# Kernel tuning notes

Measured on AMD Instinct MI355X. Metric: run time of the kernel, lower is better.

The kernel has to match this reference:

```python
import jax, jax.numpy as jnp
import numpy as np

RES = 2048
STEPS = 65536
SIGMA = 0.01
W = 32  # source computes w from sigma then hardcodes w = 32


def setup_inputs() -> dict:
    key = jax.random.key(0)
    # 3 control points (x, y) in [0, 1]
    control_points = jax.random.uniform(key, (3, 2), dtype=jnp.float32)
    return {"control_points": control_points}


def reference(control_points):
    p0, p1, p2 = control_points[0], control_points[1], control_points[2]
    # lin_interp uses torch.linspace(0, 1, steps)
    t_lin = jnp.linspace(0.0, 1.0, STEPS, dtype=jnp.float32)  # [steps]
    a = p0[:, None] + (p1 - p0)[:, None] * t_lin  # [2, steps]
    b = p1[:, None] + (p2 - p1)[:, None] * t_lin  # [2, steps]
    # forward uses arange(steps)/steps (NOT linspace) for the outer blend
    t_out = jnp.arange(STEPS, dtype=jnp.float32) / float(STEPS)
    curve = a + t_out * (b - a)  # [2, steps]

    # per-step block corner indices (int -> non-differentiable, as in torch .int())
    blocks = jnp.clip(jnp.floor(RES * curve).astype(jnp.int32) - W // 2, 0, RES - W)  # [2, steps]
    bx, by = blocks[0], blocks[1]  # [steps]
    offs = jnp.arange(W, dtype=jnp.int32)

    # grid values inside each block: self.c[a,b,t] = a/res, self.d[a,b,t] = b/res
    ci = (bx[:, None] + offs).astype(jnp.float32) / float(RES)  # [steps, w]
    cj = (by[:, None] + offs).astype(jnp.float32) / float(RES)  # [steps, w]

    dx = curve[0][:, None] - ci  # [steps, w]
    dy = curve[1][:, None] - cj  # [steps, w]
    inv = 1.0 / (2.0 * SIGMA * SIGMA)
    patch = jnp.exp(-(dx[:, :, None] ** 2 + dy[:, None, :] ** 2) * inv)  # [steps, w, w]

    # scatter each step's patch into the grid; mean over steps == sum/steps
    ii = bx[:, None, None] + offs[None, :, None]  # [steps, w, 1] -> broadcast
    jj = by[:, None, None] + offs[None, None, :]  # [steps, 1, w]
    ii = jnp.broadcast_to(ii, (STEPS, W, W))
    jj = jnp.broadcast_to(jj, (STEPS, W, W))
    raster = jnp.zeros((RES, RES), dtype=jnp.float32).at[ii, jj].add(patch)
    return raster / float(STEPS)
```

## Files before the change

kernel.cpp:

```cpp
#include <hip/hip_runtime.h>
#include <hip/hip_bf16.h>

#define RES_    2048
#define CSTEPS  128
#define TILE_   48
#define KPAD    136
#define NTHR    576

typedef _Float16 half8 __attribute__((ext_vector_type(8)));
typedef float   float4_ __attribute__((ext_vector_type(4)));

__global__ __launch_bounds__(NTHR) void bezier_scatter(const float* __restrict__ cp,
                                                       float* __restrict__ out) {
    __shared__ _Float16 sExT[TILE_][KPAD];
    __shared__ _Float16 sEyT[TILE_][KPAD];
    __shared__ float s_cx[CSTEPS], s_cy[CSTEPS];
    __shared__ int   s_bx[CSTEPS], s_by[CSTEPS];
    __shared__ int   s_Ax, s_Ay;

    const int tid = threadIdx.x;

    if (tid < CSTEPS) {
        const int gs = blockIdx.x * CSTEPS + tid;
        const float tl = (float)((double)gs / 65535.0);
        const float to = (float)gs * (1.0f / 65536.0f);
        const float p0x = cp[0], p0y = cp[1], p1x = cp[2], p1y = cp[3], p2x = cp[4], p2y = cp[5];
        const float ax = __fadd_rn(p0x, __fmul_rn(__fsub_rn(p1x, p0x), tl));
        const float ay = __fadd_rn(p0y, __fmul_rn(__fsub_rn(p1y, p0y), tl));
        const float bxf = __fadd_rn(p1x, __fmul_rn(__fsub_rn(p2x, p1x), tl));
        const float byf = __fadd_rn(p1y, __fmul_rn(__fsub_rn(p2y, p1y), tl));
        const float cx = __fadd_rn(ax, __fmul_rn(to, __fsub_rn(bxf, ax)));
        const float cy = __fadd_rn(ay, __fmul_rn(to, __fsub_rn(byf, ay)));
        const int bxi = min(max((int)floorf(__fmul_rn(2048.0f, cx)) - 16, 0), RES_ - 32);
        const int byi = min(max((int)floorf(__fmul_rn(2048.0f, cy)) - 16, 0), RES_ - 32);
        s_cx[tid] = cx; s_cy[tid] = cy; s_bx[tid] = bxi; s_by[tid] = byi;
        if (tid == 0) {
            s_Ax = min(max(bxi - 8, 0), RES_ - TILE_);
            s_Ay = min(max(byi - 8, 0), RES_ - TILE_);
        }
    }
    __syncthreads();
    const int Ax = s_Ax, Ay = s_Ay;

    for (int it = tid; it < 2 * TILE_ * (CSTEPS / 8); it += NTHR) {
        const int half_ = TILE_ * (CSTEPS / 8);
        const int table = (it >= half_);
        const int rem   = it - table * half_;
        const int o     = rem >> 4;
        const int s0    = (rem & 15) * 8;
        const float* cc = table ? s_cy : s_cx;
        const int*   bb = table ? s_by : s_bx;
        const int  base = table ? Ay : Ax;
        const float ci  = (float)(base + o) * (1.0f / 2048.0f);
        half8 v;
        #pragma unroll
        for (int j = 0; j < 8; ++j) {
            const int s = s0 + j;
            const float d = __fsub_rn(cc[s], ci);
            const float e = __expf(-__fmul_rn(__fmul_rn(d, d), 5000.0f));
            const unsigned orel = (unsigned)(base + o - bb[s]);
            v[j] = (orel < 32u) ? (_Float16)e : (_Float16)0.0f;
        }
        *(half8*)(table ? &sEyT[o][s0] : &sExT[o][s0]) = v;
    }
    __syncthreads();

    const int lane = tid & 63;
    const int wid  = tid >> 6;
    const int mt   = wid / 3, nt = wid - mt * 3;
    const int arow = mt * 16 + (lane & 15);
    const int bcol = nt * 16 + (lane & 15);
    const int kgrp = (lane >> 4) * 8;
    float4_ acc = {0.f, 0.f, 0.f, 0.f};
    #pragma unroll
    for (int kb = 0; kb < CSTEPS / 32; ++kb) {
        const half8 aF = *(const half8*)&sExT[arow][kb * 32 + kgrp];
        const half8 bF = *(const half8*)&sEyT[bcol][kb * 32 + kgrp];
        acc = __builtin_amdgcn_mfma_f32_16x16x32_f16(aF, bF, acc, 0, 0, 0);
    }

    const int coll = lane & 15;
    const int rowb = (lane >> 4) * 4;
    #pragma unroll
    for (int r = 0; r < 4; ++r) {
        const float v = acc[r];
        if (v != 0.0f) {
            const int gx = Ax + mt * 16 + rowb + r;
            const int gy = Ay + nt * 16 + coll;
            atomicAdd(&out[gx * RES_ + gy], v * (1.0f / 65536.0f));
        }
    }
}

extern "C" void kernel_launch(void* const* d_in, const int* in_sizes, int n_in,
                              void* d_out, int out_size, void* d_ws, size_t ws_size,
                              hipStream_t stream) {
    const float* cp = (const float*)d_in[0];
    float* out = (float*)d_out;
    hipMemsetAsync(out, 0, (size_t)out_size * sizeof(float), stream);
    hipLaunchKernelGGL(bezier_scatter, dim3(65536 / CSTEPS), dim3(NTHR), 0, stream, cp, out);
}
```

Baseline: 21.35 us.

## Switch from per-chunk atomic scatter to per-output-tile gather with chunk culling

Replaces the step-chunk-parallel kernel, which atomically added 48x48 patches into a memset grid, with an output-tile-parallel kernel. Each of 4096 blocks owns a 32x32 tile, culls the 512 step chunks by bounding box, and accumulates the overlapping ones with MFMA. It writes the tile directly, which removes the memset and the atomics. The cost is uneven work: blocks far from the curve only write zeros, while blocks near it loop over several chunks with repeated barriers.

After: 45.48 us. +113.0%, slower.

```diff
diff --git a/kernel.cpp b/kernel.cpp
--- a/kernel.cpp
+++ b/kernel.cpp
@@ -1,95 +1,166 @@
 #include <hip/hip_runtime.h>
 #include <hip/hip_bf16.h>
 
-#define RES_    2048
-#define CSTEPS  128
-#define TILE_   48
-#define KPAD    136
-#define NTHR    576
+#define RES_   2048
+#define CH_    128
+#define NCH    512
+#define TS_    32
+#define KPAD   136
+#define NTHR   512
 
-typedef _Float16 half8 __attribute__((ext_vector_type(8)));
+typedef _Float16 half8  __attribute__((ext_vector_type(8)));
+typedef float   float2_ __attribute__((ext_vector_type(2)));
 typedef float   float4_ __attribute__((ext_vector_type(4)));
 
-__global__ __launch_bounds__(NTHR) void bezier_scatter(const float* __restrict__ cp,
-                                                       float* __restrict__ out) {
-    __shared__ _Float16 sExT[TILE_][KPAD];
-    __shared__ _Float16 sEyT[TILE_][KPAD];
-    __shared__ float s_cx[CSTEPS], s_cy[CSTEPS];
-    __shared__ int   s_bx[CSTEPS], s_by[CSTEPS];
-    __shared__ int   s_Ax, s_Ay;
+__device__ __forceinline__ void step_eval(int gs, float p0x, float p0y, float p1x, float p1y,
+                                          float p2x, float p2y, float& cx, float& cy) {
+    const float tl = (float)((double)gs / 65535.0);
+    const float to = (float)gs * (1.0f / 65536.0f);
+    const float ax  = __fadd_rn(p0x, __fmul_rn(__fsub_rn(p1x, p0x), tl));
+    const float ay  = __fadd_rn(p0y, __fmul_rn(__fsub_rn(p1y, p0y), tl));
+    const float bxf = __fadd_rn(p1x, __fmul_rn(__fsub_rn(p2x, p1x), tl));
+    const float byf = __fadd_rn(p1y, __fmul_rn(__fsub_rn(p2y, p1y), tl));
+    cx = __fadd_rn(ax, __fmul_rn(to, __fsub_rn(bxf, ax)));
+    cy = __fadd_rn(ay, __fmul_rn(to, __fsub_rn(byf, ay)));
+}
+
+__device__ __forceinline__ void step_eval_fast(int gs, float p0x, float p0y, float p1x, float p1y,
+                                               float p2x, float p2y, float& cx, float& cy) {
+    const float tl = (float)gs * (1.0f / 65535.0f);
+    const float to = (float)gs * (1.0f / 65536.0f);
+    const float ax  = p0x + (p1x - p0x) * tl;
+    const float ay  = p0y + (p1y - p0y) * tl;
+    const float bxf = p1x + (p2x - p1x) * tl;
+    const float byf = p1y + (p2y - p1y) * tl;
+    cx = ax + to * (bxf - ax);
+    cy = ay + to * (byf - ay);
+}
+
+__global__ __launch_bounds__(NTHR) void bezier_tiles(const float* __restrict__ cp,
+                                                     float* __restrict__ out) {
+    __shared__ _Float16 sExT[TS_][KPAD];
+    __shared__ _Float16 sEyT[TS_][KPAD];
+    __shared__ float    sOut[TS_][36];
+    __shared__ float    s_cx[CH_], s_cy[CH_];
+    __shared__ int      s_bx[CH_], s_by[CH_];
+    __shared__ unsigned short s_list[NCH];
+    __shared__ int      s_wcnt[8];
+    __shared__ int      s_count;
 
     const int tid = threadIdx.x;
+    const int bid = blockIdx.x;
+    const int Tx = (bid >> 6) * TS_;
+    const int Ty = (bid & 63) * TS_;
 
-    if (tid < CSTEPS) {
-        const int gs = blockIdx.x * CSTEPS + tid;
-        const float tl = (float)((double)gs / 65535.0);
-        const float to = (float)gs * (1.0f / 65536.0f);
-        const float p0x = cp[0], p0y = cp[1], p1x = cp[2], p1y = cp[3], p2x = cp[4], p2y = cp[5];
-        const float ax = __fadd_rn(p0x, __fmul_rn(__fsub_rn(p1x, p0x), tl));
-        const float ay = __fadd_rn(p0y, __fmul_rn(__fsub_rn(p1y, p0y), tl));
-        const float bxf = __fadd_rn(p1x, __fmul_rn(__fsub_rn(p2x, p1x), tl));
-        const float byf = __fadd_rn(p1y, __fmul_rn(__fsub_rn(p2y, p1y), tl));
-        const float cx = __fadd_rn(ax, __fmul_rn(to, __fsub_rn(bxf, ax)));
-        const float cy = __fadd_rn(ay, __fmul_rn(to, __fsub_rn(byf, ay)));
-        const int bxi = min(max((int)floorf(__fmul_rn(2048.0f, cx)) - 16, 0), RES_ - 32);
-        const int byi = min(max((int)floorf(__fmul_rn(2048.0f, cy)) - 16, 0), RES_ - 32);
-        s_cx[tid] = cx; s_cy[tid] = cy; s_bx[tid] = bxi; s_by[tid] = byi;
-        if (tid == 0) {
-            s_Ax = min(max(bxi - 8, 0), RES_ - TILE_);
-            s_Ay = min(max(byi - 8, 0), RES_ - TILE_);
-        }
+    const float p0x = cp[0], p0y = cp[1], p1x = cp[2], p1y = cp[3], p2x = cp[4], p2y = cp[5];
+
+    bool ov = false;
+    {
+        float x0, y0, x1, y1;
+        step_eval_fast(tid * CH_,           p0x,p0y,p1x,p1y,p2x,p2y, x0, y0);
+        step_eval_fast(tid * CH_ + CH_ - 1, p0x,p0y,p1x,p1y,p2x,p2y, x1, y1);
+        const int bxlo = min(max((int)floorf(2048.f * fminf(x0, x1)) - 18, 0), RES_ - 32);
+        const int bxhi = min(max((int)floorf(2048.f * fmaxf(x0, x1)) - 14, 0), RES_ - 32);
+        const int bylo = min(max((int)floorf(2048.f * fminf(y0, y1)) - 18, 0), RES_ - 32);
+        const int byhi = min(max((int)floorf(2048.f * fmaxf(y0, y1)) - 14, 0), RES_ - 32);
+        ov = (bxlo <= Tx + TS_ - 1) && (bxhi + 31 >= Tx) &&
+             (bylo <= Ty + TS_ - 1) && (byhi + 31 >= Ty);
+    }
+    const unsigned long long m = __ballot(ov ? 1 : 0);
+    const int lane = tid & 63;
+    const int w    = tid >> 6;
+    if (lane == 0) s_wcnt[w] = __popcll(m);
+    __syncthreads();
+    if (ov) {
+        int pre = 0;
+        for (int i = 0; i < w; ++i) pre += s_wcnt[i];
+        const int pos = pre + __popcll(m & ((1ull << lane) - 1ull));
+        s_list[pos] = (unsigned short)tid;
+    }
+    if (tid == 0) {
+        int t = 0;
+        for (int i = 0; i < 8; ++i) t += s_wcnt[i];
+        s_count = t;
     }
     __syncthreads();
-    const int Ax = s_Ax, Ay = s_Ay;
+    const int cnt = s_count;
 
-    for (int it = tid; it < 2 * TILE_ * (CSTEPS / 8); it += NTHR) {
-        const int half_ = TILE_ * (CSTEPS / 8);
-        const int table = (it >= half_);
-        const int rem   = it - table * half_;
-        const int o     = rem >> 4;
-        const int s0    = (rem & 15) * 8;
-        const float* cc = table ? s_cy : s_cx;
-        const int*   bb = table ? s_by : s_bx;
-        const int  base = table ? Ay : Ax;
-        const float ci  = (float)(base + o) * (1.0f / 2048.0f);
-        half8 v;
+    const int orow = tid >> 4;
+    const int oc2  = (tid & 15) * 2;
+    float* const orow_ptr = &out[(size_t)(Tx + orow) * RES_ + Ty + oc2];
+
+    if (cnt == 0) {
+        *(float2_*)orow_ptr = float2_{0.f, 0.f};
+        return;
+    }
+
+    const int st = w & 3;
+    const int kh = w >> 2;
+    const int mt = st >> 1, nt = st & 1;
+    const int arow = mt * 16 + (lane & 15);
+    const int bcol = nt * 16 + (lane & 15);
+    const int kg   = kh * 64 + (lane >> 4) * 8;
+    float4_ acc = {0.f, 0.f, 0.f, 0.f};
+
+    for (int p = 0; p < cnt; ++p) {
+        const int c = s_list[p];
+        if (tid < CH_) {
+            float cx, cy;
+            step_eval(c * CH_ + tid, p0x,p0y,p1x,p1y,p2x,p2y, cx, cy);
+            s_cx[tid] = cx; s_cy[tid] = cy;
+            s_bx[tid] = min(max((int)floorf(__fmul_rn(2048.0f, cx)) - 16, 0), RES_ - 32);
+            s_by[tid] = min(max((int)floorf(__fmul_rn(2048.0f, cy)) - 16, 0), RES_ - 32);
+        }
+        __syncthreads();
         #pragma unroll
-        for (int j = 0; j < 8; ++j) {
-            const int s = s0 + j;
-            const float d = __fsub_rn(cc[s], ci);
-            const float e = __expf(-__fmul_rn(__fmul_rn(d, d), 5000.0f));
-            const unsigned orel = (unsigned)(base + o - bb[s]);
-            v[j] = (orel < 32u) ? (_Float16)e : (_Float16)0.0f;
+        for (int rep = 0; rep < 2; ++rep) {
+            const int it    = tid + rep * NTHR;
+            const int table = it >> 9;
+            const int rem   = it & 511;
+            const int o     = rem >> 4;
+            const int s0    = (rem & 15) * 8;
+            const float* cc = table ? s_cy : s_cx;
+            const int*   bb = table ? s_by : s_bx;
+            const int  base = table ? Ty : Tx;
+            const float ci  = (float)(base + o) * (1.0f / 2048.0f);
+            half8 v;
+            #pragma unroll
+            for (int j = 0; j < 8; ++j) {
+                const int s = s0 + j;
+                const float d = __fsub_rn(cc[s], ci);
+                const float e = __expf(-__fmul_rn(__fmul_rn(d, d), 5000.0f));
+                const unsigned orel = (unsigned)(base + o - bb[s]);
+                v[j] = (orel < 32u) ? (_Float16)e : (_Float16)0.0f;
+            }
+            *(half8*)(table ? &sEyT[o][s0] : &sExT[o][s0]) = v;
         }
-        *(half8*)(table ? &sEyT[o][s0] : &sExT[o][s0]) = v;
+        __syncthreads();
+        #pragma unroll
+        for (int kb = 0; kb < 2; ++kb) {
+            const int k = kb * 32 + kg;
+            const half8 aF = *(const half8*)&sExT[arow][k];
+            const half8 bF = *(const half8*)&sEyT[bcol][k];
+            acc = __builtin_amdgcn_mfma_f32_16x16x32_f16(aF, bF, acc, 0, 0, 0);
+        }
+        __syncthreads();
+    }
+
+    const float sc = 1.0f / 65536.0f;
+    const int coll = lane & 15;
+    const int rowb = (lane >> 4) * 4;
+    if (kh == 0) {
+        #pragma unroll
+        for (int r = 0; r < 4; ++r)
+            sOut[mt * 16 + rowb + r][nt * 16 + coll] = acc[r] * sc;
     }
     __syncthreads();
-
-    const int lane = tid & 63;
-    const int wid  = tid >> 6;
-    const int mt   = wid / 3, nt = wid - mt * 3;
-    const int arow = mt * 16 + (lane & 15);
-    const int bcol = nt * 16 + (lane & 15);
-    const int kgrp = (lane >> 4) * 8;
-    float4_ acc = {0.f, 0.f, 0.f, 0.f};
-    #pragma unroll
-    for (int kb = 0; kb < CSTEPS / 32; ++kb) {
-        const half8 aF = *(const half8*)&sExT[arow][kb * 32 + kgrp];
-        const half8 bF = *(const half8*)&sEyT[bcol][kb * 32 + kgrp];
-        acc = __builtin_amdgcn_mfma_f32_16x16x32_f16(aF, bF, acc, 0, 0, 0);
+    if (kh == 1) {
+        #pragma unroll
+        for (int r = 0; r < 4; ++r)
+            sOut[mt * 16 + rowb + r][nt * 16 + coll] += acc[r] * sc;
     }
-
-    const int coll = lane & 15;
-    const int rowb = (lane >> 4) * 4;
-    #pragma unroll
-    for (int r = 0; r < 4; ++r) {
-        const float v = acc[r];
-        if (v != 0.0f) {
-            const int gx = Ax + mt * 16 + rowb + r;
-            const int gy = Ay + nt * 16 + coll;
-            atomicAdd(&out[gx * RES_ + gy], v * (1.0f / 65536.0f));
-        }
-    }
+    __syncthreads();
+    *(float2_*)orow_ptr = *(const float2_*)&sOut[orow][oc2];
 }
 
 extern "C" void kernel_launch(void* const* d_in, const int* in_sizes, int n_in,
@@ -97,6 +168,5 @@
                               hipStream_t stream) {
     const float* cp = (const float*)d_in[0];
     float* out = (float*)d_out;
-    hipMemsetAsync(out, 0, (size_t)out_size * sizeof(float), stream);
-    hipLaunchKernelGGL(bezier_scatter, dim3(65536 / CSTEPS), dim3(NTHR), 0, stream, cp, out);
+    hipLaunchKernelGGL(bezier_tiles, dim3(4096), dim3(NTHR), 0, stream, cp, out);
 }
```

## Replace memset plus atomic scatter with chunk tiles and a gather pass

Applied to the files above, without the earlier changes.

Each chunk block now writes its 48x48 partial tile and its tile origin to workspace instead of atomically adding into the output. A second kernel gives each 32x32 output tile one block, which ballot-compacts the overlapping chunks and sums their tile values, then writes every output element once. This removes the separate 16 MB memset and the atomic contention, at the cost of an extra launch and a full-grid write plus workspace reads. There is also some leftover dead code in the prefix loop.

Measured after the change: 36.93 us. +73.0%, slower.

```diff
diff --git a/kernel.cpp b/kernel.cpp
--- a/kernel.cpp
+++ b/kernel.cpp
@@ -3,15 +3,19 @@
 
 #define RES_    2048
 #define CSTEPS  128
+#define NCH     512
 #define TILE_   48
 #define KPAD    136
-#define NTHR    576
+#define NTHR1   576
+#define WSTILE  2304
+#define NTHR2   256
 
-typedef _Float16 half8 __attribute__((ext_vector_type(8)));
+typedef _Float16 half8  __attribute__((ext_vector_type(8)));
 typedef float   float4_ __attribute__((ext_vector_type(4)));
 
-__global__ __launch_bounds__(NTHR) void bezier_scatter(const float* __restrict__ cp,
-                                                       float* __restrict__ out) {
+__global__ __launch_bounds__(NTHR1) void bezier_chunks(const float* __restrict__ cp,
+                                                       float* __restrict__ wst,
+                                                       int* __restrict__ wsa) {
     __shared__ _Float16 sExT[TILE_][KPAD];
     __shared__ _Float16 sEyT[TILE_][KPAD];
     __shared__ float s_cx[CSTEPS], s_cy[CSTEPS];
@@ -37,12 +41,14 @@
         if (tid == 0) {
             s_Ax = min(max(bxi - 8, 0), RES_ - TILE_);
             s_Ay = min(max(byi - 8, 0), RES_ - TILE_);
+            wsa[2 * blockIdx.x]     = s_Ax;
+            wsa[2 * blockIdx.x + 1] = s_Ay;
         }
     }
     __syncthreads();
     const int Ax = s_Ax, Ay = s_Ay;
 
-    for (int it = tid; it < 2 * TILE_ * (CSTEPS / 8); it += NTHR) {
+    for (int it = tid; it < 2 * TILE_ * (CSTEPS / 8); it += NTHR1) {
         const int half_ = TILE_ * (CSTEPS / 8);
         const int table = (it >= half_);
         const int rem   = it - table * half_;
@@ -79,17 +85,84 @@
         acc = __builtin_amdgcn_mfma_f32_16x16x32_f16(aF, bF, acc, 0, 0, 0);
     }
 
+    float* wt = wst + (size_t)blockIdx.x * WSTILE;
     const int coll = lane & 15;
     const int rowb = (lane >> 4) * 4;
     #pragma unroll
-    for (int r = 0; r < 4; ++r) {
-        const float v = acc[r];
-        if (v != 0.0f) {
-            const int gx = Ax + mt * 16 + rowb + r;
-            const int gy = Ay + nt * 16 + coll;
-            atomicAdd(&out[gx * RES_ + gy], v * (1.0f / 65536.0f));
+    for (int r = 0; r < 4; ++r)
+        wt[(mt * 16 + rowb + r) * TILE_ + nt * 16 + coll] = acc[r] * (1.0f / 65536.0f);
+}
+
+__global__ __launch_bounds__(NTHR2) void bezier_gather(const float* __restrict__ wst,
+                                                       const int* __restrict__ wsa,
+                                                       float* __restrict__ out) {
+    __shared__ unsigned short s_c[NCH];
+    __shared__ short s_ax[NCH], s_ay[NCH];
+    __shared__ int s_wcnt[8];
+    __shared__ int s_cnt;
+
+    const int tid = threadIdx.x;
+    const int bid = blockIdx.x;
+    const int Tx = (bid >> 6) * 32;
+    const int Ty = (bid & 63) * 32;
+    const int lane = tid & 63;
+    const int w = tid >> 6;
+    const unsigned long long below = (lane == 63) ? ~0ull >> 1 : (1ull << lane) - 1ull;
+
+    bool ovr[2]; unsigned long long mr[2]; int axr[2], ayr[2];
+    #pragma unroll
+    for (int r = 0; r < 2; ++r) {
+        const int c = r * 256 + tid;
+        axr[r] = wsa[2 * c]; ayr[r] = wsa[2 * c + 1];
+        ovr[r] = (axr[r] <= Tx + 31) && (axr[r] + TILE_ - 1 >= Tx) &&
+                 (ayr[r] <= Ty + 31) && (ayr[r] + TILE_ - 1 >= Ty);
+        mr[r] = __ballot(ovr[r] ? 1 : 0);
+        if (lane == 0) s_wcnt[r * 4 + w] = __popcll(mr[r]);
+    }
+    __syncthreads();
+    {
+        int tot = 0, pre[2];
+        for (int i = 0; i < 8; ++i) {
+            const int rr = i >> 2, ww = i & 3;
+            if (rr * 4 + ww == 0 * 4 + w && rr == 0) {}
+            if (i == 0 * 4 + w + 0) {}
+            tot += 0;
+        }
+        int total = 0;
+        for (int i = 0; i < 8; ++i) total += s_wcnt[i];
+        #pragma unroll
+        for (int r = 0; r < 2; ++r) {
+            int base = 0;
+            for (int i = 0; i < r * 4 + w; ++i) base += s_wcnt[i];
+            if (ovr[r]) {
+                const int pos = base + __popcll(mr[r] & ((1ull << lane) - 1ull));
+                s_c[pos]  = (unsigned short)(r * 256 + tid);
+                s_ax[pos] = (short)axr[r];
+                s_ay[pos] = (short)ayr[r];
+            }
+        }
+        if (tid == 0) s_cnt = total;
+    }
+    __syncthreads();
+
+    const int cnt = s_cnt;
+    const int row = tid >> 3;
+    const int c0  = (tid & 7) * 4;
+    const int gx  = Tx + row;
+    float4_ acc = {0.f, 0.f, 0.f, 0.f};
+    for (int p = 0; p < cnt; ++p) {
+        const int rr = gx - (int)s_ax[p];
+        if ((unsigned)rr < (unsigned)TILE_) {
+            const float* wrow = wst + (size_t)s_c[p] * WSTILE + rr * TILE_;
+            const int cc = Ty + c0 - (int)s_ay[p];
+            #pragma unroll
+            for (int i = 0; i < 4; ++i) {
+                const int ci = cc + i;
+                if ((unsigned)ci < (unsigned)TILE_) acc[i] += wrow[ci];
+            }
         }
     }
+    *(float4_*)&out[(size_t)gx * RES_ + Ty + c0] = acc;
 }
 
 extern "C" void kernel_launch(void* const* d_in, const int* in_sizes, int n_in,
@@ -97,6 +170,9 @@
                               hipStream_t stream) {
     const float* cp = (const float*)d_in[0];
     float* out = (float*)d_out;
-    hipMemsetAsync(out, 0, (size_t)out_size * sizeof(float), stream);
-    hipLaunchKernelGGL(bezier_scatter, dim3(65536 / CSTEPS), dim3(NTHR), 0, stream, cp, out);
+    float* wst = (float*)d_ws;
+    int*   wsa = (int*)((char*)d_ws + (size_t)NCH * WSTILE * 4);
+
+    hipLaunchKernelGGL(bezier_chunks, dim3(NCH), dim3(NTHR1), 0, stream, cp, wst, wsa);
+    hipLaunchKernelGGL(bezier_gather, dim3(4096), dim3(NTHR2), 0, stream, wst, wsa, out);
 }
```
